# Optimization experiments

Measured on AMD Instinct MI355X. Metric: run time of the kernel, lower is better.

The kernel has to match this reference:

```python
import jax, jax.numpy as jnp
import numpy as np

B, L = 8, 2048
Q_IN, V_IN, QK, VD = 512, 1024, 96, 96


def _conv1d_same(x_bcl, w_oik, b_o):
    # x: (B, C, L), w: (O, I, K), 'same' padding, stride 1
    y = jax.lax.conv_general_dilated(
        x_bcl, w_oik, window_strides=(1,), padding='SAME',
        dimension_numbers=('NCH', 'OIH', 'NCH'))
    return y + b_o[None, :, None]


def masked_softmax(scores, seqlengths):
    # scores: (B, L, L); mask key positions >= seqlengths[b]
    mask = jnp.arange(scores.shape[-1])[None, None, :] < seqlengths[:, None, None]
    scores = jnp.where(mask, scores, jnp.float32(-1e6))
    return jax.nn.softmax(scores, axis=-1)


def setup_inputs() -> dict:
    key = jax.random.key(0)
    ks = jax.random.split(key, 12)
    def lin(k, fan_in, shape):
        bound = 1.0 / np.sqrt(fan_in)
        return jax.random.uniform(k, shape, jnp.float32, -bound, bound)
    return {
        'plm_embedding': jax.random.normal(ks[0], (B, L, V_IN), jnp.float32),
        'evo_local': jax.random.normal(ks[1], (B, L, Q_IN), jnp.float32),
        'seqlengths': jax.random.randint(ks[2], (B,), 1, L + 1),
        'q_w': lin(ks[3], Q_IN, (QK, Q_IN)), 'q_b': lin(ks[4], Q_IN, (QK,)),
        'k_w': lin(ks[5], Q_IN + 2 * VD, (QK, Q_IN + 2 * VD)), 'k_b': lin(ks[6], Q_IN + 2 * VD, (QK,)),
        'v_w': lin(ks[7], V_IN, (VD, V_IN)), 'v_b': lin(ks[8], V_IN, (VD,)),
        'cn3_w': lin(ks[9], Q_IN * 3, (QK, Q_IN, 3)), 'cn3_b': lin(ks[9], Q_IN * 3, (QK,)),
        'cn5_w': lin(ks[10], Q_IN * 5, (QK, Q_IN, 5)), 'cn5_b': lin(ks[11], Q_IN * 5, (QK,)),
    }


def reference(plm_embedding, evo_local, seqlengths, q_w, q_b, k_w, k_b, v_w, v_b,
              cn3_w, cn3_b, cn5_w, cn5_b):
    norm = jnp.float32(1.0 / np.sqrt(QK))
    Q = jnp.einsum('bld,od->blo', evo_local, q_w) + q_b          # (B,L,QK)
    x_bcl = jnp.transpose(evo_local, (0, 2, 1))                  # (B,C,L)
    k3 = _conv1d_same(x_bcl, cn3_w, cn3_b)                       # (B,QK,L)
    k5 = _conv1d_same(x_bcl, cn5_w, cn5_b)
    cat = jnp.concatenate(
        (evo_local, jnp.transpose(k3, (0, 2, 1)), jnp.transpose(k5, (0, 2, 1))), axis=2)
    K = jnp.einsum('bld,od->blo', cat, k_w) + k_b                # (B,L,QK)
    V = jnp.einsum('bld,od->blo', plm_embedding, v_w) + v_b      # (B,L,VD)
    scores = jnp.einsum('bqd,bkd->bqk', Q, K) * norm             # (B,L,L)
    atten = masked_softmax(scores, seqlengths)
    out = jnp.einsum('bqk,bkd->bqd', atten, V)
    return out + V
```

## Files before the change

kernel.cpp:

```cpp
#include <hip/hip_runtime.h>

typedef unsigned short u16;
typedef unsigned int u32;
typedef float f32x4 __attribute__((ext_vector_type(4)));
typedef short s16x8 __attribute__((ext_vector_type(8)));

#define LSEQ 2048
#define QIN 512
#define VIN 1024
#define KCAT 704
#define KEFF 2560
#define NORMS 0.10206207261596575f

__device__ __forceinline__ u16 f2bf(float f) {
  u32 u = __float_as_uint(f);
  u = (u + 0x7fffu + ((u >> 16) & 1u)) >> 16;
  return (u16)u;
}
__device__ __forceinline__ float bf2f(u16 v) {
  return __uint_as_float(((u32)v) << 16);
}

__device__ __forceinline__ s16x8 load8cvt(const float* __restrict__ p) {
  float4 a = *(const float4*)p;
  float4 b = *(const float4*)(p + 4);
  s16x8 r;
  r[0] = (short)f2bf(a.x); r[1] = (short)f2bf(a.y);
  r[2] = (short)f2bf(a.z); r[3] = (short)f2bf(a.w);
  r[4] = (short)f2bf(b.x); r[5] = (short)f2bf(b.y);
  r[6] = (short)f2bf(b.z); r[7] = (short)f2bf(b.w);
  return r;
}

__device__ __forceinline__ s16x8 cvt2x4(float4 a, float4 b) {
  s16x8 r;
  r[0] = (short)f2bf(a.x); r[1] = (short)f2bf(a.y);
  r[2] = (short)f2bf(a.z); r[3] = (short)f2bf(a.w);
  r[4] = (short)f2bf(b.x); r[5] = (short)f2bf(b.y);
  r[6] = (short)f2bf(b.z); r[7] = (short)f2bf(b.w);
  return r;
}

__device__ __forceinline__ size_t wfrag_idx(int o, int k) {
  int kc = k >> 5, kg = (k >> 3) & 3, j = k & 7;
  int nt = o >> 4, ln = o & 15;
  return ((size_t)(kc * 6 + nt) * 64 + kg * 16 + ln) * 8 + j;
}

__global__ __launch_bounds__(256) void prep1(
    const float* __restrict__ q_w, const float* __restrict__ k_w,
    const float* __restrict__ k_b, const float* __restrict__ v_w,
    const float* __restrict__ cn3_w, const float* __restrict__ cn3_b,
    const float* __restrict__ cn5_w, const float* __restrict__ cn5_b,
    float* __restrict__ c3t, float* __restrict__ c5t,
    u16* __restrict__ qwf, u16* __restrict__ vwf,
    u16* __restrict__ kw3f, u16* __restrict__ kw5f,
    float* __restrict__ beff) {
  int blk = blockIdx.x, tid = threadIdx.x;
  if (blk < 576) {
    int idx = blk * 256 + tid;
    int t = idx / (512 * 96);
    int rem = idx - t * 512 * 96;
    int c = rem / 96, j = rem - c * 96;
    c3t[idx] = cn3_w[(j * 512 + c) * 3 + t];
  } else if (blk < 1536) {
    int idx = (blk - 576) * 256 + tid;
    int t = idx / (512 * 96);
    int rem = idx - t * 512 * 96;
    int c = rem / 96, j = rem - c * 96;
    c5t[idx] = cn5_w[(j * 512 + c) * 5 + t];
  } else if (blk < 1728) {
    int e = (blk - 1536) * 256 + tid;
    int o = e >> 9, k = e & 511;
    qwf[wfrag_idx(o, k)] = f2bf(q_w[e]);
  } else if (blk < 2112) {
    int e = (blk - 1728) * 256 + tid;
    int o = e >> 10, k = e & 1023;
    vwf[wfrag_idx(o, k)] = f2bf(v_w[e]);
  } else if (blk < 2184) {
    int e = (blk - 2112) * 256 + tid;
    int half = e / 9216;
    int i = e - half * 9216;
    int o = i / 96, j = i - o * 96;
    float v = k_w[o * KCAT + (half ? 608 : 512) + j];
    size_t di = ((size_t)((j >> 5) * 6 + (o >> 4)) * 64 +
                 ((j >> 3) & 3) * 16 + (o & 15)) * 8 + (j & 7);
    (half ? kw5f : kw3f)[di] = f2bf(v);
  } else {
    if (tid < 96) {
      const float* kwo = k_w + tid * KCAT;
      float b = k_b[tid];
      for (int j = 0; j < 96; ++j)
        b += kwo[512 + j] * cn3_b[j] + kwo[608 + j] * cn5_b[j];
      beff[tid] = b;
    }
  }
}

__global__ __launch_bounds__(256) void prep2(
    const float* __restrict__ c3t, const float* __restrict__ c5t,
    const u16* __restrict__ kw3f, const u16* __restrict__ kw5f,
    const float* __restrict__ k_w, u16* __restrict__ wefff) {
  __shared__ float Ls[4][16][100];
  int blk = blockIdx.x, tid = threadIdx.x;
  int wid = tid >> 6, lane = tid & 63, ln = lane & 15, kg = lane >> 4;
  int k = blk * 64 + wid * 16 + ln;
  bool c3ok = (k >= 512) && (k < 2048);
  const float* a5 = c5t + (size_t)k * 96;
  const float* a3 = c3t + (size_t)(c3ok ? k - 512 : 0) * 96;
  f32x4 acc[6];
  #pragma unroll
  for (int nt = 0; nt < 6; ++nt) acc[nt] = (f32x4){0.f, 0.f, 0.f, 0.f};
  #pragma unroll
  for (int jc = 0; jc < 3; ++jc) {
    s16x8 aa5 = load8cvt(a5 + jc * 32 + kg * 8);
    s16x8 aa3 = (s16x8){0, 0, 0, 0, 0, 0, 0, 0};
    if (c3ok) aa3 = load8cvt(a3 + jc * 32 + kg * 8);
    const u16* b5 = kw5f + (size_t)jc * 3072 + lane * 8;
    const u16* b3 = kw3f + (size_t)jc * 3072 + lane * 8;
    #pragma unroll
    for (int nt = 0; nt < 6; ++nt) {
      acc[nt] = __builtin_amdgcn_mfma_f32_16x16x32_bf16(
          aa5, *(const s16x8*)&b5[nt * 512], acc[nt], 0, 0, 0);
      acc[nt] = __builtin_amdgcn_mfma_f32_16x16x32_bf16(
          aa3, *(const s16x8*)&b3[nt * 512], acc[nt], 0, 0, 0);
    }
  }
  #pragma unroll
  for (int nt = 0; nt < 6; ++nt)
    #pragma unroll
    for (int r = 0; r < 4; ++r)
      Ls[wid][kg * 4 + r][nt * 16 + ln] = acc[nt][r];
  asm volatile("s_waitcnt lgkmcnt(0)" ::: "memory");
  #pragma unroll
  for (int sl = 0; sl < 3; ++sl) {
    int slot = sl * 64 + lane;
    int o = slot >> 1, rc = slot & 1;
    int k0 = blk * 64 + wid * 16 + rc * 8;
    int t = k0 >> 9, cbase = k0 & 511;
    s16x8 ov;
    #pragma unroll
    for (int e = 0; e < 8; ++e) {
      float v = Ls[wid][rc * 8 + e][o];
      if (t == 2) v += k_w[o * KCAT + cbase + e];
      ov[e] = (short)f2bf(v);
    }
    *(s16x8*)&wefff[((size_t)((k0 >> 5) * 6 + (o >> 4)) * 64 +
                     ((k0 >> 3) & 3) * 16 + (o & 15)) * 8] = ov;
  }
}

__global__ __launch_bounds__(256, 2) void proj_fused(
    const float* __restrict__ evo, const float* __restrict__ plm,
    const u16* __restrict__ qwf, const u16* __restrict__ vwf,
    const u16* __restrict__ wefff, const float* __restrict__ q_b,
    const float* __restrict__ beff, const float* __restrict__ v_b,
    u16* __restrict__ Qf, u16* __restrict__ Kf,
    u16* __restrict__ Vfr, u16* __restrict__ Vb) {
  __shared__ u16 At[2 * 68 * 72];
  __shared__ u16 LBS[18432];
  float* Ls = (float*)LBS;
  int bxr = blockIdx.x, bb = blockIdx.y;
  int tid = threadIdx.x;
  int wid = tid >> 6, lane = tid & 63, ln = lane & 15, kg = lane >> 4;
  int srow = tid >> 2, spart = tid & 3;

  if (bxr < 32) {
    int bx = bxr;
    int r0 = bx * 64;
    const float* xb = evo + (size_t)bb * LSEQ * QIN;
    bool halo = tid < 16;
    int hrow = 64 + (tid >> 2);

    float4 ra0, ra1, ra2, ra3, rb0, rb1, rb2, rb3;
    auto LOADS = [&](int s) {
      int g = r0 - 2 + srow;
      if (g >= 0 && g < LSEQ) {
        const float* p = xb + (size_t)g * QIN + s * 64 + spart * 16;
        ra0 = *(const float4*)p;       ra1 = *(const float4*)(p + 4);
        ra2 = *(const float4*)(p + 8); ra3 = *(const float4*)(p + 12);
      } else {
        ra0 = ra1 = ra2 = ra3 = make_float4(0.f, 0.f, 0.f, 0.f);
      }
      if (halo) {
        int g2 = r0 - 2 + hrow;
        if (g2 < LSEQ) {
          const float* p = xb + (size_t)g2 * QIN + s * 64 + spart * 16;
          rb0 = *(const float4*)p;       rb1 = *(const float4*)(p + 4);
          rb2 = *(const float4*)(p + 8); rb3 = *(const float4*)(p + 12);
        } else {
          rb0 = rb1 = rb2 = rb3 = make_float4(0.f, 0.f, 0.f, 0.f);
        }
      }
    };
    auto WRITES = [&](int buf) {
      u16* d = &At[(buf * 68 + srow) * 72 + spart * 16];
      *(s16x8*)d = cvt2x4(ra0, ra1);
      *(s16x8*)(d + 8) = cvt2x4(ra2, ra3);
      if (halo) {
        u16* d2 = &At[(buf * 68 + hrow) * 72 + spart * 16];
        *(s16x8*)d2 = cvt2x4(rb0, rb1);
        *(s16x8*)(d2 + 8) = cvt2x4(rb2, rb3);
      }
    };

    s16x8 br[9];
    auto LOADB = [&](int kcg) {
      #pragma unroll
      for (int j = 0; j < 9; ++j) {
        int idx = tid + j * 256;
        int chunk = idx / 384;
        int off = idx - chunk * 384;
        const u16* src = (chunk == 0)
            ? qwf + (size_t)kcg * 3072 + off * 8
            : wefff + (size_t)(chunk - 1) * 49152 + (size_t)kcg * 3072 + off * 8;
        br[j] = *(const s16x8*)src;
      }
    };
    auto STOREB = [&]() {
      #pragma unroll
      for (int j = 0; j < 9; ++j) {
        int idx = tid + j * 256;
        *(s16x8*)&LBS[idx * 8] = br[j];
      }
    };

    f32x4 accQ[6], accK[6];
    #pragma unroll
    for (int nt = 0; nt < 6; ++nt) {
      accQ[nt] = (f32x4){0.f, 0.f, 0.f, 0.f};
      accK[nt] = (f32x4){0.f, 0.f, 0.f, 0.f};
    }

    LOADS(0);
    LOADB(0);
    WRITES(0);
    STOREB();
    __syncthreads();
    int cur = 0;
    for (int s = 0; s < 8; ++s) {
      if (s < 7) LOADS(s + 1);
      #pragma unroll
      for (int cc = 0; cc < 2; ++cc) {
        int kcg = s * 2 + cc;
        bool havenext = kcg < 15;
        if (havenext) LOADB(kcg + 1);
        const u16* arow = &At[(cur * 68 + wid * 16 + ln) * 72 + cc * 32 + kg * 8];
        s16x8 aQ  = *(const s16x8*)&arow[2 * 72];
        s16x8 aK0 = *(const s16x8*)&arow[0];
        s16x8 aK1 = *(const s16x8*)&arow[1 * 72];
        s16x8 aK3 = *(const s16x8*)&arow[3 * 72];
        s16x8 aK4 = *(const s16x8*)&arow[4 * 72];
        const u16* lb = LBS + lane * 8;
        s16x8 bfr[6];
        #pragma unroll
        for (int i = 0; i < 6; ++i)
          bfr[i] = *(const s16x8*)&lb[i * 512];
        #pragma unroll
        for (int i = 0; i < 6; ++i)
          accQ[i] = __builtin_amdgcn_mfma_f32_16x16x32_bf16(
              aQ, bfr[i], accQ[i], 0, 0, 0);
        #pragma unroll
        for (int t = 0; t < 5; ++t) {
          s16x8 bf2[6];
          #pragma unroll
          for (int i = 0; i < 6; ++i)
            bf2[i] = *(const s16x8*)&lb[(1 + t) * 3072 + i * 512];
          s16x8 aK = (t == 0) ? aK0 : (t == 1) ? aK1 : (t == 2) ? aQ
                   : (t == 3) ? aK3 : aK4;
          #pragma unroll
          for (int i = 0; i < 6; ++i)
            accK[i] = __builtin_amdgcn_mfma_f32_16x16x32_bf16(
                aK, bf2[i], accK[i], 0, 0, 0);
        }
        __syncthreads();
        if (havenext) STOREB();
        if (cc == 1 && s < 7) WRITES(cur ^ 1);
        __syncthreads();
      }
      if (s < 7) cur ^= 1;
    }

    size_t qt = (size_t)bb * 128 + bx * 4 + wid;
    #pragma unroll
    for (int nt = 0; nt < 6; ++nt)
      #pragma unroll
      for (int r = 0; r < 4; ++r)
        Ls[wid * 1600 + (kg * 4 + r) * 100 + nt * 16 + ln] = accQ[nt][r];
    asm volatile("s_waitcnt lgkmcnt(0)" ::: "memory");
    #pragma unroll
    for (int sl = 0; sl < 3; ++sl) {
      int slot = sl * 64 + lane;
      int r = slot / 12, cg = slot % 12;
      s16x8 ov;
      #pragma unroll
      for (int e = 0; e < 8; ++e) {
        int c = cg * 8 + e;
        ov[e] = (short)f2bf(Ls[wid * 1600 + r * 100 + c] + q_b[c]);
      }
      *(s16x8*)&Qf[((qt * 3 + (cg >> 2)) * 64 + (cg & 3) * 16 + r) * 8] = ov;
    }
    asm volatile("s_waitcnt lgkmcnt(0) vmcnt(0)" ::: "memory");
    #pragma unroll
    for (int nt = 0; nt < 6; ++nt)
      #pragma unroll
      for (int r = 0; r < 4; ++r)
        Ls[wid * 1600 + (kg * 4 + r) * 100 + nt * 16 + ln] = accK[nt][r];
    asm volatile("s_waitcnt lgkmcnt(0)" ::: "memory");
    #pragma unroll
    for (int sl = 0; sl < 3; ++sl) {
      int slot = sl * 64 + lane;
      int r = slot / 12, cg = slot % 12;
      s16x8 ov;
      #pragma unroll
      for (int e = 0; e < 8; ++e) {
        int c = cg * 8 + e;
        ov[e] = (short)f2bf(Ls[wid * 1600 + r * 100 + c] + beff[c]);
      }
      *(s16x8*)&Kf[((qt * 3 + (cg >> 2)) * 64 + (cg & 3) * 16 + r) * 8] = ov;
    }
  } else {
    int bx = bxr - 32;
    const float* xb = plm + ((size_t)bb * LSEQ + bx * 64) * VIN;
    float4 ra0, ra1, ra2, ra3;
    auto LOADS = [&](int s) {
      const float* p = xb + (size_t)srow * VIN + s * 64 + spart * 16;
      ra0 = *(const float4*)p;       ra1 = *(const float4*)(p + 4);
      ra2 = *(const float4*)(p + 8); ra3 = *(const float4*)(p + 12);
    };
    auto WRITES = [&](int buf) {
      u16* d = &At[(buf * 68 + srow) * 72 + spart * 16];
      *(s16x8*)d = cvt2x4(ra0, ra1);
      *(s16x8*)(d + 8) = cvt2x4(ra2, ra3);
    };
    s16x8 br[3];
    auto LOADB = [&](int s) {
      #pragma unroll
      for (int j = 0; j < 3; ++j) {
        int idx = tid + j * 256;
        br[j] = *(const s16x8*)(vwf + (size_t)s * 6144 + idx * 8);
      }
    };
    auto STOREB = [&]() {
      #pragma unroll
      for (int j = 0; j < 3; ++j) {
        int idx = tid + j * 256;
        *(s16x8*)&LBS[idx * 8] = br[j];
      }
    };

    f32x4 acc[6];
    #pragma unroll
    for (int nt = 0; nt < 6; ++nt) acc[nt] = (f32x4){0.f, 0.f, 0.f, 0.f};

    LOADS(0);
    LOADB(0);
    WRITES(0);
    STOREB();
    __syncthreads();
    int cur = 0;
    for (int s = 0; s < 16; ++s) {
      if (s < 15) {
        LOADS(s + 1);
        LOADB(s + 1);
      }
      #pragma unroll
      for (int cc = 0; cc < 2; ++cc) {
        s16x8 a = *(const s16x8*)&At[(cur * 68 + wid * 16 + ln) * 72 +
                                     cc * 32 + kg * 8];
        const u16* lb = LBS + cc * 3072 + lane * 8;
        s16x8 bfr[6];
        #pragma unroll
        for (int nt = 0; nt < 6; ++nt)
          bfr[nt] = *(const s16x8*)&lb[nt * 512];
        #pragma unroll
        for (int nt = 0; nt < 6; ++nt)
          acc[nt] = __builtin_amdgcn_mfma_f32_16x16x32_bf16(
              a, bfr[nt], acc[nt], 0, 0, 0);
      }
      __syncthreads();
      if (s < 15) {
        STOREB();
        WRITES(cur ^ 1);
      }
      __syncthreads();
      if (s < 15) cur ^= 1;
    }

    #pragma unroll
    for (int nt = 0; nt < 6; ++nt)
      #pragma unroll
      for (int r = 0; r < 4; ++r)
        Ls[wid * 1600 + (kg * 4 + r) * 100 + nt * 16 + ln] = acc[nt][r];
    asm volatile("s_waitcnt lgkmcnt(0)" ::: "memory");
    #pragma unroll
    for (int sl = 0; sl < 3; ++sl) {
      int slot = sl * 64 + lane;
      int r = slot / 12, cg = slot % 12;
      s16x8 ov;
      #pragma unroll
      for (int e = 0; e < 8; ++e) {
        int c = cg * 8 + e;
        ov[e] = (short)f2bf(Ls[wid * 1600 + r * 100 + c] + v_b[c]);
      }
      *(s16x8*)&Vb[((size_t)bb * LSEQ + bx * 64 + wid * 16 + r) * 96 + cg * 8] = ov;
    }
    #pragma unroll
    for (int sl = 0; sl < 3; ++sl) {
      int slot = sl * 64 + lane;
      int c = slot >> 1, rc = slot & 1;
      int key0 = bx * 64 + wid * 16 + rc * 8;
      s16x8 fv;
      #pragma unroll
      for (int e = 0; e < 8; ++e)
        fv[e] = (short)f2bf(Ls[wid * 1600 + (rc * 8 + e) * 100 + c] + v_b[c]);
      *(s16x8*)&Vfr[(((size_t)bb * 64 + (key0 >> 5)) * 6 + (c >> 4)) * 512 +
                    (((key0 >> 3) & 3) * 16 + (c & 15)) * 8] = fv;
    }
  }
}

__global__ __launch_bounds__(256, 4) void attn_kernel(
    const u16* __restrict__ Qf, const u16* __restrict__ Kf,
    const u16* __restrict__ Vfr, const u16* __restrict__ Vb,
    const int* __restrict__ seqlen, float* __restrict__ out) {
  __shared__ u16 Ps[4][16][40];
  __shared__ float Cacc[4][16][97];
  __shared__ float Cml[4][16][2];

  int bid = blockIdx.x;
  int bb = (bid >> 3) & 7;
  int bx = ((bid >> 6) << 3) | (bid & 7);
  int tid = threadIdx.x;
  int wid = tid >> 6, lane = tid & 63, ln = lane & 15, kg = lane >> 4;
  int n = seqlen[bb];
  int nkc = (n + 31) >> 5;

  size_t qt = (size_t)bb * 128 + bx;
  s16x8 aQ[3];
  #pragma unroll
  for (int kk = 0; kk < 3; ++kk)
    aQ[kk] = *(const s16x8*)&Qf[((qt * 3 + kk) * 64 + lane) * 8];

  float m[4], lsum[4];
  f32x4 acc[6];
  #pragma unroll
  for (int r = 0; r < 4; ++r) { m[r] = -1e30f; lsum[r] = 0.f; }
  #pragma unroll
  for (int nt = 0; nt < 6; ++nt) acc[nt] = (f32x4){0.f, 0.f, 0.f, 0.f};

  const u16* Kbb = Kf + (size_t)bb * 128 * 1536;
  s16x8 kf[6];
  {
    int k0 = (wid < nkc) ? wid : 0;
    const u16* kp = Kbb + (size_t)k0 * 3072 + lane * 8;
    #pragma unroll
    for (int i = 0; i < 6; ++i) kf[i] = *(const s16x8*)&kp[i * 512];
  }

  for (int kc = wid; kc < nkc; kc += 4) {
    int key0 = kc * 32;
    f32x4 s0 = (f32x4){0.f, 0.f, 0.f, 0.f};
    f32x4 s1 = (f32x4){0.f, 0.f, 0.f, 0.f};
    #pragma unroll
    for (int kk = 0; kk < 3; ++kk) {
      s0 = __builtin_amdgcn_mfma_f32_16x16x32_bf16(aQ[kk], kf[kk], s0, 0, 0, 0);
      s1 = __builtin_amdgcn_mfma_f32_16x16x32_bf16(aQ[kk], kf[3 + kk], s1, 0, 0, 0);
    }

    s16x8 kf2[6];
    {
      int kn = (kc + 4 < nkc) ? kc + 4 : 0;
      const u16* kp = Kbb + (size_t)kn * 3072 + lane * 8;
      #pragma unroll
      for (int i = 0; i < 6; ++i) kf2[i] = *(const s16x8*)&kp[i * 512];
    }

    bool v0 = (key0 + ln) < n;
    bool v1 = (key0 + 16 + ln) < n;
    float sv0[4], sv1[4], mx[4];
    #pragma unroll
    for (int r = 0; r < 4; ++r) {
      sv0[r] = v0 ? s0[r] * NORMS : -1e30f;
      sv1[r] = v1 ? s1[r] * NORMS : -1e30f;
      mx[r] = fmaxf(sv0[r], sv1[r]);
    }
    #pragma unroll
    for (int r = 0; r < 4; ++r) {
      mx[r] = fmaxf(mx[r], __shfl_xor(mx[r], 1, 16));
      mx[r] = fmaxf(mx[r], __shfl_xor(mx[r], 2, 16));
      mx[r] = fmaxf(mx[r], __shfl_xor(mx[r], 4, 16));
      mx[r] = fmaxf(mx[r], __shfl_xor(mx[r], 8, 16));
    }
    float p0[4], p1[4], rs[4];
    bool defer = __all((mx[0] <= m[0] + 8.f) && (mx[1] <= m[1] + 8.f) &&
                       (mx[2] <= m[2] + 8.f) && (mx[3] <= m[3] + 8.f));
    if (defer) {
      #pragma unroll
      for (int r = 0; r < 4; ++r) {
        p0[r] = __expf(sv0[r] - m[r]);
        p1[r] = __expf(sv1[r] - m[r]);
        rs[r] = p0[r] + p1[r];
      }
      #pragma unroll
      for (int r = 0; r < 4; ++r) {
        rs[r] += __shfl_xor(rs[r], 1, 16);
        rs[r] += __shfl_xor(rs[r], 2, 16);
        rs[r] += __shfl_xor(rs[r], 4, 16);
        rs[r] += __shfl_xor(rs[r], 8, 16);
        lsum[r] += rs[r];
      }
    } else {
      float fac[4];
      #pragma unroll
      for (int r = 0; r < 4; ++r) {
        float mn = fmaxf(m[r], mx[r]);
        fac[r] = __expf(m[r] - mn);
        p0[r] = __expf(sv0[r] - mn);
        p1[r] = __expf(sv1[r] - mn);
        rs[r] = p0[r] + p1[r];
        m[r] = mn;
      }
      #pragma unroll
      for (int r = 0; r < 4; ++r) {
        rs[r] += __shfl_xor(rs[r], 1, 16);
        rs[r] += __shfl_xor(rs[r], 2, 16);
        rs[r] += __shfl_xor(rs[r], 4, 16);
        rs[r] += __shfl_xor(rs[r], 8, 16);
        lsum[r] = lsum[r] * fac[r] + rs[r];
      }
      #pragma unroll
      for (int nt = 0; nt < 6; ++nt)
        #pragma unroll
        for (int r = 0; r < 4; ++r) acc[nt][r] *= fac[r];
    }

    u16* Pw = &Ps[wid][0][0];
    #pragma unroll
    for (int r = 0; r < 4; ++r) {
      Pw[(kg * 4 + r) * 40 + ln] = f2bf(p0[r]);
      Pw[(kg * 4 + r) * 40 + 16 + ln] = f2bf(p1[r]);
    }
    s16x8 pa = *(const s16x8*)&Pw[ln * 40 + kg * 8];

    const u16* vf = Vfr + (((size_t)bb * 64 + kc) * 6 * 64) * 8 + lane * 8;
    #pragma unroll
    for (int nt = 0; nt < 6; ++nt) {
      s16x8 bv = *(const s16x8*)&vf[(size_t)nt * 512];
      acc[nt] = __builtin_amdgcn_mfma_f32_16x16x32_bf16(pa, bv, acc[nt], 0, 0, 0);
    }
    #pragma unroll
    for (int i = 0; i < 6; ++i) kf[i] = kf2[i];
  }

  #pragma unroll
  for (int nt = 0; nt < 6; ++nt)
    #pragma unroll
    for (int r = 0; r < 4; ++r)
      Cacc[wid][kg * 4 + r][nt * 16 + ln] = acc[nt][r];
  if (ln == 0) {
    #pragma unroll
    for (int r = 0; r < 4; ++r) {
      Cml[wid][kg * 4 + r][0] = m[r];
      Cml[wid][kg * 4 + r][1] = lsum[r];
    }
  }
  __syncthreads();

  size_t obase = ((size_t)bb * LSEQ + bx * 16) * 96;
  for (int i = tid; i < 1536; i += 256) {
    int row = i / 96;
    float mg = -1e30f;
    #pragma unroll
    for (int w = 0; w < 4; ++w) mg = fmaxf(mg, Cml[w][row][0]);
    float lg = 0.f, av = 0.f;
    #pragma unroll
    for (int w = 0; w < 4; ++w) {
      float e = __expf(Cml[w][row][0] - mg);
      lg += Cml[w][row][1] * e;
      av += Cacc[w][row][i - row * 96] * e;
    }
    out[obase + i] = av / lg + bf2f(Vb[obase + i]);
  }
}

extern "C" void kernel_launch(void* const* d_in, const int* in_sizes, int n_in,
                              void* d_out, int out_size, void* d_ws,
                              size_t ws_size, hipStream_t stream) {
  const float* plm   = (const float*)d_in[0];
  const float* evo   = (const float*)d_in[1];
  const int* seqlen  = (const int*)d_in[2];
  const float* q_w   = (const float*)d_in[3];
  const float* q_b   = (const float*)d_in[4];
  const float* k_w   = (const float*)d_in[5];
  const float* k_b   = (const float*)d_in[6];
  const float* v_w   = (const float*)d_in[7];
  const float* v_b   = (const float*)d_in[8];
  const float* cn3_w = (const float*)d_in[9];
  const float* cn3_b = (const float*)d_in[10];
  const float* cn5_w = (const float*)d_in[11];
  const float* cn5_b = (const float*)d_in[12];

  char* ws = (char*)d_ws;
  u16* wefff  = (u16*)(ws + 0);
  float* beff = (float*)(ws + 491520);
  u16* qwf    = (u16*)(ws + 492032);
  u16* vwf    = (u16*)(ws + 590336);
  float* c3t  = (float*)(ws + 786944);
  float* c5t  = (float*)(ws + 1376768);
  u16* kw3f   = (u16*)(ws + 2359808);
  u16* kw5f   = (u16*)(ws + 2378240);
  u16* Qf     = (u16*)(ws + 2396672);
  u16* Kf     = (u16*)(ws + 5542400);
  u16* Vfr    = (u16*)(ws + 8688128);
  u16* Vb     = (u16*)(ws + 11833856);
  float* out  = (float*)d_out;

  prep1<<<2185, 256, 0, stream>>>(q_w, k_w, k_b, v_w, cn3_w, cn3_b, cn5_w,
                                  cn5_b, c3t, c5t, qwf, vwf, kw3f, kw5f, beff);
  prep2<<<40, 256, 0, stream>>>(c3t, c5t, kw3f, kw5f, k_w, wefff);
  proj_fused<<<dim3(64, 8), 256, 0, stream>>>(evo, plm, qwf, vwf, wefff,
                                              q_b, beff, v_b, Qf, Kf, Vfr, Vb);
  attn_kernel<<<1024, 256, 0, stream>>>(Qf, Kf, Vfr, Vb, seqlen, out);
}
```

Measured before the change: 85.81 us.

## Double rows per block in projection kernel to reuse weight tiles

The fused projection kernel now gives each block 128 rows instead of 64, and each wave computes two 16-row M-tiles that share the same B fragments loaded from shared memory. The grid is halved to 32x8. This halves the per-row weight traffic into LDS and the halo overhead. In exchange it uses more accumulator registers and shared memory, and with only 256 blocks there are fewer blocks per CU on the 256-CU MI355X, which can lower occupancy and latency hiding.

```diff
diff --git a/kernel.cpp b/kernel.cpp
--- a/kernel.cpp
+++ b/kernel.cpp
@@ -157,80 +157,95 @@
     const float* __restrict__ beff, const float* __restrict__ v_b,
     u16* __restrict__ Qf, u16* __restrict__ Kf,
     u16* __restrict__ Vfr, u16* __restrict__ Vb) {
-  __shared__ u16 At[2 * 68 * 72];
+  __shared__ u16 At[2 * 132 * 72];
   __shared__ u16 LBS[18432];
   float* Ls = (float*)LBS;
   int bxr = blockIdx.x, bb = blockIdx.y;
   int tid = threadIdx.x;
   int wid = tid >> 6, lane = tid & 63, ln = lane & 15, kg = lane >> 4;
-  int srow = tid >> 2, spart = tid & 3;
-
-  if (bxr < 32) {
+  int spart = tid & 3;
+  int arow = tid >> 2;
+
+  if (bxr < 16) {
     int bx = bxr;
-    int r0 = bx * 64;
+    int r0 = bx * 128;
     const float* xb = evo + (size_t)bb * LSEQ * QIN;
-    bool halo = tid < 16;
-    int hrow = 64 + (tid >> 2);
-
-    float4 ra0, ra1, ra2, ra3, rb0, rb1, rb2, rb3;
+
+    float4 qa0, qa1, qa2, qa3, qb0, qb1, qb2, qb3, qc0, qc1, qc2, qc3;
     auto LOADS = [&](int s) {
-      int g = r0 - 2 + srow;
-      if (g >= 0 && g < LSEQ) {
-        const float* p = xb + (size_t)g * QIN + s * 64 + spart * 16;
-        ra0 = *(const float4*)p;       ra1 = *(const float4*)(p + 4);
-        ra2 = *(const float4*)(p + 8); ra3 = *(const float4*)(p + 12);
+      int ga = r0 - 2 + arow;
+      if (ga >= 0 && ga < LSEQ) {
+        const float* p = xb + (size_t)ga * QIN + s * 64 + spart * 16;
+        qa0 = *(const float4*)p;       qa1 = *(const float4*)(p + 4);
+        qa2 = *(const float4*)(p + 8); qa3 = *(const float4*)(p + 12);
       } else {
-        ra0 = ra1 = ra2 = ra3 = make_float4(0.f, 0.f, 0.f, 0.f);
-      }
-      if (halo) {
-        int g2 = r0 - 2 + hrow;
-        if (g2 < LSEQ) {
-          const float* p = xb + (size_t)g2 * QIN + s * 64 + spart * 16;
-          rb0 = *(const float4*)p;       rb1 = *(const float4*)(p + 4);
-          rb2 = *(const float4*)(p + 8); rb3 = *(const float4*)(p + 12);
+        qa0 = qa1 = qa2 = qa3 = make_float4(0.f, 0.f, 0.f, 0.f);
+      }
+      int gb = ga + 64;
+      if (gb < LSEQ) {
+        const float* p = xb + (size_t)gb * QIN + s * 64 + spart * 16;
+        qb0 = *(const float4*)p;       qb1 = *(const float4*)(p + 4);
+        qb2 = *(const float4*)(p + 8); qb3 = *(const float4*)(p + 12);
+      } else {
+        qb0 = qb1 = qb2 = qb3 = make_float4(0.f, 0.f, 0.f, 0.f);
+      }
+      if (tid < 16) {
+        int gc = r0 - 2 + 128 + arow;
+        if (gc < LSEQ) {
+          const float* p = xb + (size_t)gc * QIN + s * 64 + spart * 16;
+          qc0 = *(const float4*)p;       qc1 = *(const float4*)(p + 4);
+          qc2 = *(const float4*)(p + 8); qc3 = *(const float4*)(p + 12);
         } else {
-          rb0 = rb1 = rb2 = rb3 = make_float4(0.f, 0.f, 0.f, 0.f);
+          qc0 = qc1 = qc2 = qc3 = make_float4(0.f, 0.f, 0.f, 0.f);
         }
       }
     };
     auto WRITES = [&](int buf) {
-      u16* d = &At[(buf * 68 + srow) * 72 + spart * 16];
-      *(s16x8*)d = cvt2x4(ra0, ra1);
-      *(s16x8*)(d + 8) = cvt2x4(ra2, ra3);
-      if (halo) {
-        u16* d2 = &At[(buf * 68 + hrow) * 72 + spart * 16];
-        *(s16x8*)d2 = cvt2x4(rb0, rb1);
-        *(s16x8*)(d2 + 8) = cvt2x4(rb2, rb3);
-      }
-    };
-
-    s16x8 br[9];
+      u16* d = &At[(buf * 132 + arow) * 72 + spart * 16];
+      *(s16x8*)d = cvt2x4(qa0, qa1);
+      *(s16x8*)(d + 8) = cvt2x4(qa2, qa3);
+      u16* d2 = &At[(buf * 132 + 64 + arow) * 72 + spart * 16];
+      *(s16x8*)d2 = cvt2x4(qb0, qb1);
+      *(s16x8*)(d2 + 8) = cvt2x4(qb2, qb3);
+      if (tid < 16) {
+        u16* d3 = &At[(buf * 132 + 128 + arow) * 72 + spart * 16];
+        *(s16x8*)d3 = cvt2x4(qc0, qc1);
+        *(s16x8*)(d3 + 8) = cvt2x4(qc2, qc3);
+      }
+    };
+
+    s16x8 br0, br1, br2, br3, br4, br5, br6, br7, br8;
     auto LOADB = [&](int kcg) {
-      #pragma unroll
-      for (int j = 0; j < 9; ++j) {
-        int idx = tid + j * 256;
-        int chunk = idx / 384;
-        int off = idx - chunk * 384;
-        const u16* src = (chunk == 0)
-            ? qwf + (size_t)kcg * 3072 + off * 8
-            : wefff + (size_t)(chunk - 1) * 49152 + (size_t)kcg * 3072 + off * 8;
-        br[j] = *(const s16x8*)src;
-      }
+      #define LB(j, dst)                                                     \
+        {                                                                    \
+          int idx = tid + j * 256;                                           \
+          int chunk = idx / 384;                                             \
+          int off = idx - chunk * 384;                                       \
+          const u16* src = (chunk == 0)                                      \
+              ? qwf + (size_t)kcg * 3072 + off * 8                           \
+              : wefff + (size_t)(chunk - 1) * 49152 + (size_t)kcg * 3072 +   \
+                    off * 8;                                                 \
+          dst = *(const s16x8*)src;                                          \
+        }
+      LB(0, br0) LB(1, br1) LB(2, br2) LB(3, br3) LB(4, br4)
+      LB(5, br5) LB(6, br6) LB(7, br7) LB(8, br8)
+      #undef LB
     };
     auto STOREB = [&]() {
-      #pragma unroll
-      for (int j = 0; j < 9; ++j) {
-        int idx = tid + j * 256;
-        *(s16x8*)&LBS[idx * 8] = br[j];
-      }
-    };
-
-    f32x4 accQ[6], accK[6];
-    #pragma unroll
-    for (int nt = 0; nt < 6; ++nt) {
-      accQ[nt] = (f32x4){0.f, 0.f, 0.f, 0.f};
-      accK[nt] = (f32x4){0.f, 0.f, 0.f, 0.f};
-    }
+      #define SB(j, src) *(s16x8*)&LBS[(tid + j * 256) * 8] = src;
+      SB(0, br0) SB(1, br1) SB(2, br2) SB(3, br3) SB(4, br4)
+      SB(5, br5) SB(6, br6) SB(7, br7) SB(8, br8)
+      #undef SB
+    };
+
+    f32x4 accQ[2][6], accK[2][6];
+    #pragma unroll
+    for (int mr = 0; mr < 2; ++mr)
+      #pragma unroll
+      for (int nt = 0; nt < 6; ++nt) {
+        accQ[mr][nt] = (f32x4){0.f, 0.f, 0.f, 0.f};
+        accK[mr][nt] = (f32x4){0.f, 0.f, 0.f, 0.f};
+      }
 
     LOADS(0);
     LOADB(0);
@@ -245,33 +260,54 @@
         int kcg = s * 2 + cc;
         bool havenext = kcg < 15;
         if (havenext) LOADB(kcg + 1);
-        const u16* arow = &At[(cur * 68 + wid * 16 + ln) * 72 + cc * 32 + kg * 8];
-        s16x8 aQ  = *(const s16x8*)&arow[2 * 72];
-        s16x8 aK0 = *(const s16x8*)&arow[0];
-        s16x8 aK1 = *(const s16x8*)&arow[1 * 72];
-        s16x8 aK3 = *(const s16x8*)&arow[3 * 72];
-        s16x8 aK4 = *(const s16x8*)&arow[4 * 72];
+        const u16* ar0 = &At[(cur * 132 + wid * 32 + ln) * 72 + cc * 32 + kg * 8];
+        const u16* ar1 = ar0 + 16 * 72;
         const u16* lb = LBS + lane * 8;
-        s16x8 bfr[6];
-        #pragma unroll
-        for (int i = 0; i < 6; ++i)
-          bfr[i] = *(const s16x8*)&lb[i * 512];
-        #pragma unroll
-        for (int i = 0; i < 6; ++i)
-          accQ[i] = __builtin_amdgcn_mfma_f32_16x16x32_bf16(
-              aQ, bfr[i], accQ[i], 0, 0, 0);
+        {
+          s16x8 aq0 = *(const s16x8*)&ar0[2 * 72];
+          s16x8 aq1 = *(const s16x8*)&ar1[2 * 72];
+          s16x8 bq0 = *(const s16x8*)&lb[0 * 512];
+          s16x8 bq1 = *(const s16x8*)&lb[1 * 512];
+          s16x8 bq2 = *(const s16x8*)&lb[2 * 512];
+          s16x8 bq3 = *(const s16x8*)&lb[3 * 512];
+          s16x8 bq4 = *(const s16x8*)&lb[4 * 512];
+          s16x8 bq5 = *(const s16x8*)&lb[5 * 512];
+          accQ[0][0] = __builtin_amdgcn_mfma_f32_16x16x32_bf16(aq0, bq0, accQ[0][0], 0, 0, 0);
+          accQ[0][1] = __builtin_amdgcn_mfma_f32_16x16x32_bf16(aq0, bq1, accQ[0][1], 0, 0, 0);
+          accQ[0][2] = __builtin_amdgcn_mfma_f32_16x16x32_bf16(aq0, bq2, accQ[0][2], 0, 0, 0);
+          accQ[0][3] = __builtin_amdgcn_mfma_f32_16x16x32_bf16(aq0, bq3, accQ[0][3], 0, 0, 0);
+          accQ[0][4] = __builtin_amdgcn_mfma_f32_16x16x32_bf16(aq0, bq4, accQ[0][4], 0, 0, 0);
+          accQ[0][5] = __builtin_amdgcn_mfma_f32_16x16x32_bf16(aq0, bq5, accQ[0][5], 0, 0, 0);
+          accQ[1][0] = __builtin_amdgcn_mfma_f32_16x16x32_bf16(aq1, bq0, accQ[1][0], 0, 0, 0);
+          accQ[1][1] = __builtin_amdgcn_mfma_f32_16x16x32_bf16(aq1, bq1, accQ[1][1], 0, 0, 0);
+          accQ[1][2] = __builtin_amdgcn_mfma_f32_16x16x32_bf16(aq1, bq2, accQ[1][2], 0, 0, 0);
+          accQ[1][3] = __builtin_amdgcn_mfma_f32_16x16x32_bf16(aq1, bq3, accQ[1][3], 0, 0, 0);
+          accQ[1][4] = __builtin_amdgcn_mfma_f32_16x16x32_bf16(aq1, bq4, accQ[1][4], 0, 0, 0);
+          accQ[1][5] = __builtin_amdgcn_mfma_f32_16x16x32_bf16(aq1, bq5, accQ[1][5], 0, 0, 0);
+        }
         #pragma unroll
         for (int t = 0; t < 5; ++t) {
-          s16x8 bf2[6];
-          #pragma unroll
-          for (int i = 0; i < 6; ++i)
-            bf2[i] = *(const s16x8*)&lb[(1 + t) * 3072 + i * 512];
-          s16x8 aK = (t == 0) ? aK0 : (t == 1) ? aK1 : (t == 2) ? aQ
-                   : (t == 3) ? aK3 : aK4;
-          #pragma unroll
-          for (int i = 0; i < 6; ++i)
-            accK[i] = __builtin_amdgcn_mfma_f32_16x16x32_bf16(
-                aK, bf2[i], accK[i], 0, 0, 0);
+          s16x8 ak0 = *(const s16x8*)&ar0[t * 72];
+          s16x8 ak1 = *(const s16x8*)&ar1[t * 72];
+          const u16* lk = lb + (1 + t) * 3072;
+          s16x8 bk0 = *(const s16x8*)&lk[0 * 512];
+          s16x8 bk1 = *(const s16x8*)&lk[1 * 512];
+          s16x8 bk2 = *(const s16x8*)&lk[2 * 512];
+          s16x8 bk3 = *(const s16x8*)&lk[3 * 512];
+          s16x8 bk4 = *(const s16x8*)&lk[4 * 512];
+          s16x8 bk5 = *(const s16x8*)&lk[5 * 512];
+          accK[0][0] = __builtin_amdgcn_mfma_f32_16x16x32_bf16(ak0, bk0, accK[0][0], 0, 0, 0);
+          accK[0][1] = __builtin_amdgcn_mfma_f32_16x16x32_bf16(ak0, bk1, accK[0][1], 0, 0, 0);
+          accK[0][2] = __builtin_amdgcn_mfma_f32_16x16x32_bf16(ak0, bk2, accK[0][2], 0, 0, 0);
+          accK[0][3] = __builtin_amdgcn_mfma_f32_16x16x32_bf16(ak0, bk3, accK[0][3], 0, 0, 0);
+          accK[0][4] = __builtin_amdgcn_mfma_f32_16x16x32_bf16(ak0, bk4, accK[0][4], 0, 0, 0);
+          accK[0][5] = __builtin_amdgcn_mfma_f32_16x16x32_bf16(ak0, bk5, accK[0][5], 0, 0, 0);
+          accK[1][0] = __builtin_amdgcn_mfma_f32_16x16x32_bf16(ak1, bk0, accK[1][0], 0, 0, 0);
+          accK[1][1] = __builtin_amdgcn_mfma_f32_16x16x32_bf16(ak1, bk1, accK[1][1], 0, 0, 0);
+          accK[1][2] = __builtin_amdgcn_mfma_f32_16x16x32_bf16(ak1, bk2, accK[1][2], 0, 0, 0);
+          accK[1][3] = __builtin_amdgcn_mfma_f32_16x16x32_bf16(ak1, bk3, accK[1][3], 0, 0, 0);
+          accK[1][4] = __builtin_amdgcn_mfma_f32_16x16x32_bf16(ak1, bk4, accK[1][4], 0, 0, 0);
+          accK[1][5] = __builtin_amdgcn_mfma_f32_16x16x32_bf16(ak1, bk5, accK[1][5], 0, 0, 0);
         }
         __syncthreads();
         if (havenext) STOREB();
@@ -281,77 +317,85 @@
       if (s < 7) cur ^= 1;
     }
 
-    size_t qt = (size_t)bb * 128 + bx * 4 + wid;
-    #pragma unroll
-    for (int nt = 0; nt < 6; ++nt)
-      #pragma unroll
-      for (int r = 0; r < 4; ++r)
-        Ls[wid * 1600 + (kg * 4 + r) * 100 + nt * 16 + ln] = accQ[nt][r];
-    asm volatile("s_waitcnt lgkmcnt(0)" ::: "memory");
-    #pragma unroll
-    for (int sl = 0; sl < 3; ++sl) {
-      int slot = sl * 64 + lane;
-      int r = slot / 12, cg = slot % 12;
-      s16x8 ov;
-      #pragma unroll
-      for (int e = 0; e < 8; ++e) {
-        int c = cg * 8 + e;
-        ov[e] = (short)f2bf(Ls[wid * 1600 + r * 100 + c] + q_b[c]);
-      }
-      *(s16x8*)&Qf[((qt * 3 + (cg >> 2)) * 64 + (cg & 3) * 16 + r) * 8] = ov;
-    }
-    asm volatile("s_waitcnt lgkmcnt(0) vmcnt(0)" ::: "memory");
-    #pragma unroll
-    for (int nt = 0; nt < 6; ++nt)
-      #pragma unroll
-      for (int r = 0; r < 4; ++r)
-        Ls[wid * 1600 + (kg * 4 + r) * 100 + nt * 16 + ln] = accK[nt][r];
-    asm volatile("s_waitcnt lgkmcnt(0)" ::: "memory");
-    #pragma unroll
-    for (int sl = 0; sl < 3; ++sl) {
-      int slot = sl * 64 + lane;
-      int r = slot / 12, cg = slot % 12;
-      s16x8 ov;
-      #pragma unroll
-      for (int e = 0; e < 8; ++e) {
-        int c = cg * 8 + e;
-        ov[e] = (short)f2bf(Ls[wid * 1600 + r * 100 + c] + beff[c]);
-      }
-      *(s16x8*)&Kf[((qt * 3 + (cg >> 2)) * 64 + (cg & 3) * 16 + r) * 8] = ov;
+    #pragma unroll
+    for (int mr = 0; mr < 2; ++mr) {
+      size_t qt = (size_t)bb * 128 + bx * 8 + wid * 2 + mr;
+      #pragma unroll
+      for (int nt = 0; nt < 6; ++nt)
+        #pragma unroll
+        for (int r = 0; r < 4; ++r)
+          Ls[wid * 1600 + (kg * 4 + r) * 100 + nt * 16 + ln] = accQ[mr][nt][r];
+      asm volatile("s_waitcnt lgkmcnt(0)" ::: "memory");
+      #pragma unroll
+      for (int sl = 0; sl < 3; ++sl) {
+        int slot = sl * 64 + lane;
+        int r = slot / 12, cg = slot % 12;
+        s16x8 ov;
+        #pragma unroll
+        for (int e = 0; e < 8; ++e) {
+          int c = cg * 8 + e;
+          ov[e] = (short)f2bf(Ls[wid * 1600 + r * 100 + c] + q_b[c]);
+        }
+        *(s16x8*)&Qf[((qt * 3 + (cg >> 2)) * 64 + (cg & 3) * 16 + r) * 8] = ov;
+      }
+      asm volatile("s_waitcnt lgkmcnt(0)" ::: "memory");
+      #pragma unroll
+      for (int nt = 0; nt < 6; ++nt)
+        #pragma unroll
+        for (int r = 0; r < 4; ++r)
+          Ls[wid * 1600 + (kg * 4 + r) * 100 + nt * 16 + ln] = accK[mr][nt][r];
+      asm volatile("s_waitcnt lgkmcnt(0)" ::: "memory");
+      #pragma unroll
+      for (int sl = 0; sl < 3; ++sl) {
+        int slot = sl * 64 + lane;
+        int r = slot / 12, cg = slot % 12;
+        s16x8 ov;
+        #pragma unroll
+        for (int e = 0; e < 8; ++e) {
+          int c = cg * 8 + e;
+          ov[e] = (short)f2bf(Ls[wid * 1600 + r * 100 + c] + beff[c]);
+        }
+        *(s16x8*)&Kf[((qt * 3 + (cg >> 2)) * 64 + (cg & 3) * 16 + r) * 8] = ov;
+      }
+      asm volatile("s_waitcnt lgkmcnt(0)" ::: "memory");
     }
   } else {
-    int bx = bxr - 32;
-    const float* xb = plm + ((size_t)bb * LSEQ + bx * 64) * VIN;
-    float4 ra0, ra1, ra2, ra3;
+    int bx = bxr - 16;
+    const float* xb = plm + ((size_t)bb * LSEQ + bx * 128) * VIN;
+    float4 qa0, qa1, qa2, qa3, qb0, qb1, qb2, qb3;
     auto LOADS = [&](int s) {
-      const float* p = xb + (size_t)srow * VIN + s * 64 + spart * 16;
-      ra0 = *(const float4*)p;       ra1 = *(const float4*)(p + 4);
-      ra2 = *(const float4*)(p + 8); ra3 = *(const float4*)(p + 12);
+      const float* p = xb + (size_t)arow * VIN + s * 64 + spart * 16;
+      qa0 = *(const float4*)p;       qa1 = *(const float4*)(p + 4);
+      qa2 = *(const float4*)(p + 8); qa3 = *(const float4*)(p + 12);
+      const float* p2 = p + (size_t)64 * VIN;
+      qb0 = *(const float4*)p2;       qb1 = *(const float4*)(p2 + 4);
+      qb2 = *(const float4*)(p2 + 8); qb3 = *(const float4*)(p2 + 12);
     };
     auto WRITES = [&](int buf) {
-      u16* d = &At[(buf * 68 + srow) * 72 + spart * 16];
-      *(s16x8*)d = cvt2x4(ra0, ra1);
-      *(s16x8*)(d + 8) = cvt2x4(ra2, ra3);
-    };
-    s16x8 br[3];
+      u16* d = &At[(buf * 132 + arow) * 72 + spart * 16];
+      *(s16x8*)d = cvt2x4(qa0, qa1);
+      *(s16x8*)(d + 8) = cvt2x4(qa2, qa3);
+      u16* d2 = &At[(buf * 132 + 64 + arow) * 72 + spart * 16];
+      *(s16x8*)d2 = cvt2x4(qb0, qb1);
+      *(s16x8*)(d2 + 8) = cvt2x4(qb2, qb3);
+    };
+    s16x8 br0, br1, br2;
     auto LOADB = [&](int s) {
-      #pragma unroll
-      for (int j = 0; j < 3; ++j) {
-        int idx = tid + j * 256;
-        br[j] = *(const s16x8*)(vwf + (size_t)s * 6144 + idx * 8);
-      }
+      br0 = *(const s16x8*)(vwf + (size_t)s * 6144 + (tid + 0) * 8);
+      br1 = *(const s16x8*)(vwf + (size_t)s * 6144 + (tid + 256) * 8);
+      br2 = *(const s16x8*)(vwf + (size_t)s * 6144 + (tid + 512) * 8);
     };
     auto STOREB = [&]() {
-      #pragma unroll
-      for (int j = 0; j < 3; ++j) {
-        int idx = tid + j * 256;
-        *(s16x8*)&LBS[idx * 8] = br[j];
-      }
-    };
-
-    f32x4 acc[6];
-    #pragma unroll
-    for (int nt = 0; nt < 6; ++nt) acc[nt] = (f32x4){0.f, 0.f, 0.f, 0.f};
+      *(s16x8*)&LBS[(tid + 0) * 8] = br0;
+      *(s16x8*)&LBS[(tid + 256) * 8] = br1;
+      *(s16x8*)&LBS[(tid + 512) * 8] = br2;
+    };
+
+    f32x4 acc[2][6];
+    #pragma unroll
+    for (int mr = 0; mr < 2; ++mr)
+      #pragma unroll
+      for (int nt = 0; nt < 6; ++nt) acc[mr][nt] = (f32x4){0.f, 0.f, 0.f, 0.f};
 
     LOADS(0);
     LOADB(0);
@@ -366,17 +410,28 @@
       }
       #pragma unroll
       for (int cc = 0; cc < 2; ++cc) {
-        s16x8 a = *(const s16x8*)&At[(cur * 68 + wid * 16 + ln) * 72 +
-                                     cc * 32 + kg * 8];
+        const u16* ap = &At[(cur * 132 + wid * 32 + ln) * 72 + cc * 32 + kg * 8];
+        s16x8 a0 = *(const s16x8*)&ap[0];
+        s16x8 a1 = *(const s16x8*)&ap[16 * 72];
         const u16* lb = LBS + cc * 3072 + lane * 8;
-        s16x8 bfr[6];
-        #pragma unroll
-        for (int nt = 0; nt < 6; ++nt)
-          bfr[nt] = *(const s16x8*)&lb[nt * 512];
-        #pragma unroll
-        for (int nt = 0; nt < 6; ++nt)
-          acc[nt] = __builtin_amdgcn_mfma_f32_16x16x32_bf16(
-              a, bfr[nt], acc[nt], 0, 0, 0);
+        s16x8 b0 = *(const s16x8*)&lb[0 * 512];
+        s16x8 b1 = *(const s16x8*)&lb[1 * 512];
+        s16x8 b2 = *(const s16x8*)&lb[2 * 512];
+        s16x8 b3 = *(const s16x8*)&lb[3 * 512];
+        s16x8 b4 = *(const s16x8*)&lb[4 * 512];
+        s16x8 b5 = *(const s16x8*)&lb[5 * 512];
+        acc[0][0] = __builtin_amdgcn_mfma_f32_16x16x32_bf16(a0, b0, acc[0][0], 0, 0, 0);
+        acc[0][1] = __builtin_amdgcn_mfma_f32_16x16x32_bf16(a0, b1, acc[0][1], 0, 0, 0);
+        acc[0][2] = __builtin_amdgcn_mfma_f32_16x16x32_bf16(a0, b2, acc[0][2], 0, 0, 0);
+        acc[0][3] = __builtin_amdgcn_mfma_f32_16x16x32_bf16(a0, b3, acc[0][3], 0, 0, 0);
+        acc[0][4] = __builtin_amdgcn_mfma_f32_16x16x32_bf16(a0, b4, acc[0][4], 0, 0, 0);
+        acc[0][5] = __builtin_amdgcn_mfma_f32_16x16x32_bf16(a0, b5, acc[0][5], 0, 0, 0);
+        acc[1][0] = __builtin_amdgcn_mfma_f32_16x16x32_bf16(a1, b0, acc[1][0], 0, 0, 0);
+        acc[1][1] = __builtin_amdgcn_mfma_f32_16x16x32_bf16(a1, b1, acc[1][1], 0, 0, 0);
+        acc[1][2] = __builtin_amdgcn_mfma_f32_16x16x32_bf16(a1, b2, acc[1][2], 0, 0, 0);
+        acc[1][3] = __builtin_amdgcn_mfma_f32_16x16x32_bf16(a1, b3, acc[1][3], 0, 0, 0);
+        acc[1][4] = __builtin_amdgcn_mfma_f32_16x16x32_bf16(a1, b4, acc[1][4], 0, 0, 0);
+        acc[1][5] = __builtin_amdgcn_mfma_f32_16x16x32_bf16(a1, b5, acc[1][5], 0, 0, 0);
       }
       __syncthreads();
       if (s < 15) {
@@ -388,34 +443,39 @@
     }
 
     #pragma unroll
-    for (int nt = 0; nt < 6; ++nt)
-      #pragma unroll
-      for (int r = 0; r < 4; ++r)
-        Ls[wid * 1600 + (kg * 4 + r) * 100 + nt * 16 + ln] = acc[nt][r];
-    asm volatile("s_waitcnt lgkmcnt(0)" ::: "memory");
-    #pragma unroll
-    for (int sl = 0; sl < 3; ++sl) {
-      int slot = sl * 64 + lane;
-      int r = slot / 12, cg = slot % 12;
-      s16x8 ov;
-      #pragma unroll
-      for (int e = 0; e < 8; ++e) {
-        int c = cg * 8 + e;
-        ov[e] = (short)f2bf(Ls[wid * 1600 + r * 100 + c] + v_b[c]);
-      }
-      *(s16x8*)&Vb[((size_t)bb * LSEQ + bx * 64 + wid * 16 + r) * 96 + cg * 8] = ov;
-    }
-    #pragma unroll
-    for (int sl = 0; sl < 3; ++sl) {
-      int slot = sl * 64 + lane;
-      int c = slot >> 1, rc = slot & 1;
-      int key0 = bx * 64 + wid * 16 + rc * 8;
-      s16x8 fv;
-      #pragma unroll
-      for (int e = 0; e < 8; ++e)
-        fv[e] = (short)f2bf(Ls[wid * 1600 + (rc * 8 + e) * 100 + c] + v_b[c]);
-      *(s16x8*)&Vfr[(((size_t)bb * 64 + (key0 >> 5)) * 6 + (c >> 4)) * 512 +
-                    (((key0 >> 3) & 3) * 16 + (c & 15)) * 8] = fv;
+    for (int mr = 0; mr < 2; ++mr) {
+      #pragma unroll
+      for (int nt = 0; nt < 6; ++nt)
+        #pragma unroll
+        for (int r = 0; r < 4; ++r)
+          Ls[wid * 1600 + (kg * 4 + r) * 100 + nt * 16 + ln] = acc[mr][nt][r];
+      asm volatile("s_waitcnt lgkmcnt(0)" ::: "memory");
+      int rbase = bx * 128 + wid * 32 + mr * 16;
+      #pragma unroll
+      for (int sl = 0; sl < 3; ++sl) {
+        int slot = sl * 64 + lane;
+        int r = slot / 12, cg = slot % 12;
+        s16x8 ov;
+        #pragma unroll
+        for (int e = 0; e < 8; ++e) {
+          int c = cg * 8 + e;
+          ov[e] = (short)f2bf(Ls[wid * 1600 + r * 100 + c] + v_b[c]);
+        }
+        *(s16x8*)&Vb[((size_t)bb * LSEQ + rbase + r) * 96 + cg * 8] = ov;
+      }
+      #pragma unroll
+      for (int sl = 0; sl < 3; ++sl) {
+        int slot = sl * 64 + lane;
+        int c = slot >> 1, rc = slot & 1;
+        int key0 = rbase + rc * 8;
+        s16x8 fv;
+        #pragma unroll
+        for (int e = 0; e < 8; ++e)
+          fv[e] = (short)f2bf(Ls[wid * 1600 + (rc * 8 + e) * 100 + c] + v_b[c]);
+        *(s16x8*)&Vfr[(((size_t)bb * 64 + (key0 >> 5)) * 6 + (c >> 4)) * 512 +
+                      (((key0 >> 3) & 3) * 16 + (c & 15)) * 8] = fv;
+      }
+      asm volatile("s_waitcnt lgkmcnt(0)" ::: "memory");
     }
   }
 }
@@ -619,7 +679,7 @@
   prep1<<<2185, 256, 0, stream>>>(q_w, k_w, k_b, v_w, cn3_w, cn3_b, cn5_w,
                                   cn5_b, c3t, c5t, qwf, vwf, kw3f, kw5f, beff);
   prep2<<<40, 256, 0, stream>>>(c3t, c5t, kw3f, kw5f, k_w, wefff);
-  proj_fused<<<dim3(64, 8), 256, 0, stream>>>(evo, plm, qwf, vwf, wefff,
+  proj_fused<<<dim3(32, 8), 256, 0, stream>>>(evo, plm, qwf, vwf, wefff,
                                               q_b, beff, v_b, Qf, Kf, Vfr, Vb);
   attn_kernel<<<1024, 256, 0, stream>>>(Qf, Kf, Vfr, Vb, seqlen, out);
 }
```

Result: slower. 97.03 us (+13.1%).
